# Kernel tuning notes

Measured on AMD Instinct MI355X. Metric: run time of the kernel, lower is better.

## Reference

```python
import jax, jax.numpy as jnp
import numpy as np

B, C, H, W = 32, 384, 32, 32
NCH = 4           # chunks per branch (mixing_size = [4,4,4])
CH = C // NCH     # 96 channels per chunk


def setup_inputs() -> dict:
    key = jax.random.key(0)
    ks = iter(jax.random.split(key, 32))
    r = lambda shape, s=0.05: jax.random.normal(next(ks), shape, dtype=jnp.float32) * s
    inp = {"x": jax.random.normal(next(ks), (B, C, H, W), dtype=jnp.float32)}
    for b, k in zip((1, 2, 3), (1, 3, 5)):
        inp[f"f{b}_mlp_w1"] = r((2, CH, CH // 8))
        inp[f"f{b}_mlp_b1"] = r((2, CH // 8))
        inp[f"f{b}_mlp_w2"] = r((2, CH // 8, CH))
        inp[f"f{b}_mlp_b2"] = r((2, CH))
        inp[f"f{b}_conv_w"] = r((2, CH, 1, k, k))
        inp[f"f{b}_conv_b"] = r((2, CH))
    inp["fusion_w1"] = r((C, C // 4))
    inp["fusion_b1"] = r((C // 4,))
    inp["fusion_w2"] = r((C // 4, 3 * C))
    inp["fusion_b2"] = r((3 * C,))
    inp["proj_w"] = r((C, C))
    inp["proj_b"] = r((C,))
    return inp


def _gelu(x):
    return jax.nn.gelu(x, approximate=False)  # torch nn.GELU default (erf)


def _branch(x, mw1, mb1, mw2, mb2, cw, cb, pad):
    # x: (B, C, H, W); chunks of CH channels; even idx -> MLP (channel-last), odd -> depthwise conv
    chunks = jnp.split(x, NCH, axis=1)
    outs, mi, ci = [], 0, 0
    for i, c in enumerate(chunks):
        if i % 2 == 0:
            h = _gelu(jnp.einsum('bchw,cd->bdhw', c, mw1[mi]) + mb1[mi][:, None, None])
            y = jnp.einsum('bdhw,dc->bchw', h, mw2[mi]) + mb2[mi][:, None, None]
            mi += 1
        else:
            y = jax.lax.conv_general_dilated(
                c, cw[ci], window_strides=(1, 1), padding=[(pad, pad), (pad, pad)],
                feature_group_count=CH, dimension_numbers=('NCHW', 'OIHW', 'NCHW'))
            y = y + cb[ci][:, None, None]
            ci += 1
        outs.append(y)
    return jnp.concatenate(outs, axis=1)


def reference(x,
              f1_mlp_w1, f1_mlp_b1, f1_mlp_w2, f1_mlp_b2, f1_conv_w, f1_conv_b,
              f2_mlp_w1, f2_mlp_b1, f2_mlp_w2, f2_mlp_b2, f2_conv_w, f2_conv_b,
              f3_mlp_w1, f3_mlp_b1, f3_mlp_w2, f3_mlp_b2, f3_conv_w, f3_conv_b,
              fusion_w1, fusion_b1, fusion_w2, fusion_b2, proj_w, proj_b):
    x1 = _branch(x, f1_mlp_w1, f1_mlp_b1, f1_mlp_w2, f1_mlp_b2, f1_conv_w, f1_conv_b, pad=0)
    x2 = _branch(x, f2_mlp_w1, f2_mlp_b1, f2_mlp_w2, f2_mlp_b2, f2_conv_w, f2_conv_b, pad=1)
    x3 = _branch(x, f3_mlp_w1, f3_mlp_b1, f3_mlp_w2, f3_mlp_b2, f3_conv_w, f3_conv_b, pad=2)
    # softmax-gated multi-scale fusion
    a = (x1 + x2 + x3).mean(axis=(2, 3))                            # (B, C)
    g = _gelu(a @ fusion_w1 + fusion_b1) @ fusion_w2 + fusion_b2     # (B, 3C)
    g = g.reshape(a.shape[0], C, 3).transpose(2, 0, 1)               # (3, B, C)
    w = jax.nn.softmax(g, axis=0)[:, :, :, None, None]               # (3, B, C, 1, 1)
    comb = x1 * w[0] + x2 * w[1] + x3 * w[2]                         # (B, C, H, W)
    out = jnp.einsum('bchw,cd->bdhw', comb, proj_w) + proj_b[:, None, None]
    return out
```

## Files before the change

kernel.cpp:

```cpp
#include <hip/hip_runtime.h>
#include <math.h>

#define B_  32
#define C_  384
#define HW  1024

typedef float          f32x4 __attribute__((ext_vector_type(4)));
typedef short          s16x8 __attribute__((ext_vector_type(8)));
typedef unsigned short us8v  __attribute__((ext_vector_type(8)));

struct KParams {
  const float* x;
  const float* mw1[3]; const float* mb1[3]; const float* mw2[3]; const float* mb2[3];
  const float* cw[3];  const float* cb[3];
  const float* fw1; const float* fb1; const float* fw2; const float* fb2;
  const float* pw;  const float* pb;
  float* wg;
  float* H_part;
  float* acv_part;
  unsigned short* pwT;
  float* out;
};

__device__ __forceinline__ float gelu_exact(float v) {
  return 0.5f * v * (1.0f + erff(v * 0.70710678118654752440f));
}
__device__ __forceinline__ unsigned short f2bf(float f) {
  unsigned u = __float_as_uint(f);
  u += 0x7FFFu + ((u >> 16) & 1u);
  return (unsigned short)(u >> 16);
}
__device__ __forceinline__ float bf2f(unsigned short h) {
  return __uint_as_float(((unsigned)h) << 16);
}

__global__ __launch_bounds__(256) void k_prep(KParams P) {
  __shared__ float tile[32][33];
  const int td = blockIdx.x % 12, tc = blockIdx.x / 12;
  const int j = threadIdx.x & 31, i0 = threadIdx.x >> 5;
  const int gcoff = (tc < 3) ? 0 : (tc < 6 ? 96 : (tc < 9 ? -96 : 0));
  for (int i = i0; i < 32; i += 8)
    tile[i][j] = P.pw[(size_t)(tc*32 + i + gcoff)*C_ + td*32 + j];
  __syncthreads();
  for (int i = i0; i < 32; i += 8)
    P.pwT[(size_t)(td*32 + i)*C_ + tc*32 + j] = f2bf(tile[j][i]);
}

template<int HALF>
__device__ __forceinline__ void conv_strip(const float* xc, int h0, int row,
                                           float w1t, const float* w3, const float* w5,
                                           float* y0, float* y1, float* y2) {
#pragma unroll
  for (int p = 0; p < 16; ++p) { y0[p] = 0.f; y1[p] = 0.f; y2[p] = 0.f; }
#pragma unroll
  for (int dy = 0; dy < 5; ++dy) {
    const int hr = h0 + row - 2 + dy;
    float win[20];
    if (hr >= 0 && hr < 32) {
#pragma unroll
      for (int u = 0; u < 5; ++u)
        *(float4*)&win[u*4] = *(const float4*)&xc[hr*32 + HALF*12 + u*4];
    } else {
#pragma unroll
      for (int u = 0; u < 20; ++u) win[u] = 0.f;
    }
#pragma unroll
    for (int dx = 0; dx < 5; ++dx) {
      const float w = w5[dy*5 + dx];
#pragma unroll
      for (int p = 0; p < 16; ++p) {
        const int ri = p + dx - 2 + HALF*4;
        if (ri >= 0 && ri < 20) y2[p] += win[ri] * w;
      }
    }
    if (dy >= 1 && dy <= 3) {
#pragma unroll
      for (int dx = 0; dx < 3; ++dx) {
        const float w = w3[(dy-1)*3 + dx];
#pragma unroll
        for (int p = 0; p < 16; ++p) {
          const int ri = p + dx - 1 + HALF*4;
          if (ri >= 0 && ri < 20) y1[p] += win[ri] * w;
        }
      }
      if (dy == 2) {
#pragma unroll
        for (int p = 0; p < 16; ++p) y0[p] = win[p + HALF*4] * w1t;
      }
    }
  }
}

__global__ __launch_bounds__(256, 2) void k_sum(KParams P) {
  __shared__ __align__(16) char sm[49152 + 13824 + 256];
  const int bid = blockIdx.x;
  const int b = bid >> 5, ci = (bid >> 3) & 3, q = bid & 7;
  const int h0 = q * 4;
  const int t = threadIdx.x;

  if ((ci & 1) == 0) {
    const int mi = ci >> 1;
    float* Xl  = (float*)sm;
    float* w1l = (float*)(sm + 49152);
    float* Hl  = (float*)(sm + 49152 + 13824);
    for (int i = t; i < 3456; i += 256) {
      int s = i / 1152, r = i - s*1152;
      w1l[i] = P.mw1[s][mi*1152 + r];
    }
    for (int i = t*4; i < 12288; i += 1024) {
      int c = i >> 7, pix = i & 127;
      *(float4*)&Xl[i] = *(const float4*)&P.x[(size_t)(b*C_ + mi*192 + c)*HW + h0*32 + pix];
    }
    __syncthreads();
    const int quad = t & 31, sjg = t >> 6;
    const int cq = (t >> 5) & 1;
    const int sj0 = sjg * 9;
    float h[9][4];
#pragma unroll
    for (int u = 0; u < 9; ++u) { h[u][0]=0.f; h[u][1]=0.f; h[u][2]=0.f; h[u][3]=0.f; }
    int wbase[9];
#pragma unroll
    for (int u = 0; u < 9; ++u) {
      int sj = sj0 + u, s = sj / 12, jj = sj % 12;
      wbase[u] = s*1152 + jj;
    }
    for (int c = cq*48; c < cq*48 + 48; ++c) {
      const float4 xv = *(const float4*)&Xl[c*128 + quad*4];
#pragma unroll
      for (int u = 0; u < 9; ++u) {
        const float w = w1l[wbase[u] + c*12];
        h[u][0] += xv.x*w; h[u][1] += xv.y*w; h[u][2] += xv.z*w; h[u][3] += xv.w*w;
      }
    }
#pragma unroll
    for (int u = 0; u < 9; ++u)
#pragma unroll
      for (int p = 0; p < 4; ++p) h[u][p] += __shfl_xor(h[u][p], 32, 64);
    float hs[9];
#pragma unroll
    for (int u = 0; u < 9; ++u) {
      int sj = sj0 + u, s = sj / 12, jj = sj % 12;
      const float bias = P.mb1[s][mi*12 + jj];
      float sum = 0.f;
#pragma unroll
      for (int p = 0; p < 4; ++p) sum += gelu_exact(h[u][p] + bias);
#pragma unroll
      for (int m = 16; m >= 1; m >>= 1) sum += __shfl_xor(sum, m, 64);
      hs[u] = sum;
    }
    if ((t & 63) == 0) {
#pragma unroll
      for (int u = 0; u < 9; ++u) Hl[sj0 + u] = hs[u];
    }
    __syncthreads();
    if (t < 36) P.H_part[(size_t)((b*2 + mi)*8 + q)*36 + t] = Hl[t];
  } else {
    const int gi = ci >> 1;
    float* accl = (float*)sm;
    if (t < 96) accl[t] = 0.f;
    __syncthreads();
    for (int it = 0; it < 2; ++it) {
      const int task = t + 256*it;
      if (task < 384) {
        const int row = task & 3, cc = task >> 2;
        const int gcl = gi*96 + cc;
        const float* xc = P.x + (size_t)(b*C_ + (2*gi+1)*96 + cc)*HW;
        const float w1t = P.cw[0][gcl];
        float w3[9], w5[25];
#pragma unroll
        for (int k2 = 0; k2 < 9; ++k2)  w3[k2] = P.cw[1][gcl*9 + k2];
#pragma unroll
        for (int k2 = 0; k2 < 25; ++k2) w5[k2] = P.cw[2][gcl*25 + k2];
        float val = 0.f;
        {
          float y0[16], y1[16], y2[16];
          conv_strip<0>(xc, h0, row, w1t, w3, w5, y0, y1, y2);
#pragma unroll
          for (int p = 0; p < 16; ++p) val += y0[p] + y1[p] + y2[p];
          conv_strip<1>(xc, h0, row, w1t, w3, w5, y0, y1, y2);
#pragma unroll
          for (int p = 0; p < 16; ++p) val += y0[p] + y1[p] + y2[p];
        }
        atomicAdd(&accl[cc], val);
      }
    }
    __syncthreads();
    if (t < 96) P.acv_part[(size_t)((b*2 + gi)*8 + q)*96 + t] = accl[t];
  }
}

__global__ __launch_bounds__(128) void k_gate(KParams P) {
  const int b = blockIdx.x, t = threadIdx.x;
  __shared__ float am[C_], g1v[96], Hs[2][36];
  for (int i = t; i < 72; i += 128) {
    int mi = i / 36, sj = i % 36;
    float s = 0.f;
    for (int q = 0; q < 8; ++q) s += P.H_part[(size_t)((b*2+mi)*8 + q)*36 + sj];
    Hs[mi][sj] = s * (1.0f/1024.0f);
  }
  __syncthreads();
  for (int i = t; i < 192; i += 128) {
    int mi = i / 96, cc = i % 96;
    float a = 0.f;
    for (int s = 0; s < 3; ++s) {
      float y = P.mb2[s][mi*96 + cc];
      for (int jj = 0; jj < 12; ++jj) y += Hs[mi][s*12+jj] * P.mw2[s][mi*1152 + jj*96 + cc];
      a += y;
    }
    am[mi*192 + cc] = a;
  }
  for (int i = t; i < 192; i += 128) {
    int gi = i / 96, cc = i % 96;
    float s = 0.f;
    for (int q = 0; q < 8; ++q) s += P.acv_part[(size_t)((b*2+gi)*8 + q)*96 + cc];
    s *= (1.0f/1024.0f);
    for (int sb = 0; sb < 3; ++sb) s += P.cb[sb][gi*96 + cc];
    am[(2*gi+1)*96 + cc] = s;
  }
  __syncthreads();
  if (t < 96) {
    float acc = P.fb1[t];
    for (int c = 0; c < C_; ++c) acc += am[c] * P.fw1[c*96 + t];
    g1v[t] = gelu_exact(acc);
  }
  __syncthreads();
  for (int c = t; c < C_; c += 128) {
    float l0 = P.fb2[c*3+0], l1 = P.fb2[c*3+1], l2 = P.fb2[c*3+2];
    for (int jj = 0; jj < 96; ++jj) {
      const float g = g1v[jj];
      const float* f = P.fw2 + jj*1152 + c*3;
      l0 += g*f[0]; l1 += g*f[1]; l2 += g*f[2];
    }
    const float m = fmaxf(l0, fmaxf(l1, l2));
    const float e0 = expf(l0-m), e1 = expf(l1-m), e2 = expf(l2-m);
    const float inv = 1.0f/(e0+e1+e2);
    P.wg[0*(B_*C_) + b*C_ + c] = e0*inv;
    P.wg[1*(B_*C_) + b*C_ + c] = e1*inv;
    P.wg[2*(B_*C_) + b*C_ + c] = e2*inv;
  }
}

template<int HALF>
__device__ __forceinline__ void conv_phase(const KParams& P, int b, int h0,
                                           char* combB, const float* wgl, int tt) {
  for (int it = 0; it < 3; ++it) {
    const int tid = tt + 256*it;
    const int row = tid & 3, c192 = tid >> 2;
    const int gi = c192 / 96, cc = c192 - gi*96;
    const int gcl = gi*96 + cc;
    const int gc = (2*gi + 1)*96 + cc;
    const int kp = 192 + gi*96 + cc;
    const float* xc = P.x + (size_t)(b*C_ + gc)*HW;
    const float w1t = P.cw[0][gcl];
    float w3[9], w5[25];
#pragma unroll
    for (int k2 = 0; k2 < 9; ++k2)  w3[k2] = P.cw[1][gcl*9 + k2];
#pragma unroll
    for (int k2 = 0; k2 < 25; ++k2) w5[k2] = P.cw[2][gcl*25 + k2];
    float y0[16], y1[16], y2[16];
    conv_strip<HALF>(xc, h0, row, w1t, w3, w5, y0, y1, y2);
    const float g0 = wgl[0*C_ + gc], g1 = wgl[1*C_ + gc], g2 = wgl[2*C_ + gc];
    const float cbg = g0*P.cb[0][gcl] + g1*P.cb[1][gcl] + g2*P.cb[2][gcl];
#pragma unroll
    for (int p = 0; p < 16; ++p) {
      const float v = g0*y0[p] + g1*y1[p] + g2*y2[p] + cbg;
      const int pix = row*32 + HALF*16 + p;
      const int off = pix*768 + (((kp*2)) ^ ((pix & 15) << 4));
      *(unsigned short*)(combB + off) = f2bf(v);
    }
  }
}

__global__ __launch_bounds__(512, 1) void k_proj(KParams P) {
  __shared__ __align__(16) char smem[159744];
  char* combB = smem;
  char* hlB   = smem + 98304;
  char* XB    = smem + 116736;
  unsigned short* wlB = (unsigned short*)(smem + 141312);
  float* wgl  = (float*)(smem + 155136);

  const int t = threadIdx.x;
  const int b  = blockIdx.x >> 3;
  const int h0 = (blockIdx.x & 7) * 4;

  for (int i = t; i < 1152; i += 512)
    wgl[i] = P.wg[(size_t)(i/C_)*(B_*C_) + b*C_ + (i % C_)];
  for (int i = t; i < 6912; i += 512) {
    int s = i / 2304, r = i - s*2304, mi2 = r / 1152, rr = r - mi2*1152;
    wlB[i] = f2bf(P.mw1[s][mi2*1152 + rr]);
  }
  for (int i = t*4; i < 12288; i += 2048) {
    int c = i >> 7, pix = i & 127;
    float4 v = *(const float4*)&P.x[(size_t)(b*C_ + 0*192 + c)*HW + h0*32 + pix];
    unsigned lo = (unsigned)f2bf(v.x) | ((unsigned)f2bf(v.y) << 16);
    unsigned hi = (unsigned)f2bf(v.z) | ((unsigned)f2bf(v.w) << 16);
    *(uint2*)(XB + c*256 + pix*2) = make_uint2(lo, hi);
  }
  __syncthreads();

#pragma unroll 1
  for (int mi = 0; mi < 2; ++mi) {
    if (t < 256) {
      const int oct = t & 15, cq = (t >> 4) & 1, sjg = t >> 5;
      const int nsj = (sjg < 4) ? 5 : 4;
      const int sj0 = (sjg < 4) ? sjg*5 : 20 + (sjg - 4)*4;
      int wbase[5]; float bias[5];
#pragma unroll
      for (int u = 0; u < 5; ++u) {
        int sj = sj0 + ((u < 5 && u < nsj) ? u : 0);
        int s = sj / 12, jj = sj - s*12;
        wbase[u] = (s*2 + mi)*1152 + jj;
        bias[u] = P.mb1[s][mi*12 + jj];
      }
      float h[5][8];
#pragma unroll
      for (int u = 0; u < 5; ++u)
#pragma unroll
        for (int p = 0; p < 8; ++p) h[u][p] = 0.f;
      for (int c = cq*48; c < cq*48 + 48; ++c) {
        const us8v xv = *(const us8v*)(XB + c*256 + oct*16);
        float xf[8];
#pragma unroll
        for (int p = 0; p < 8; ++p) xf[p] = bf2f(xv[p]);
#pragma unroll
        for (int u = 0; u < 5; ++u) {
          if (u < nsj) {
            const float w = bf2f(wlB[wbase[u] + c*12]);
#pragma unroll
            for (int p = 0; p < 8; ++p) h[u][p] += xf[p]*w;
          }
        }
      }
#pragma unroll
      for (int u = 0; u < 5; ++u)
#pragma unroll
        for (int p = 0; p < 8; ++p) h[u][p] += __shfl_xor(h[u][p], 16, 64);
      if (cq == 0) {
#pragma unroll
        for (int u = 0; u < 5; ++u) {
          if (u < nsj) {
            us8v o;
#pragma unroll
            for (int p = 0; p < 8; ++p) o[p] = f2bf(gelu_exact(h[u][p] + bias[u]));
            *(us8v*)(hlB + (mi*36 + sj0 + u)*256 + oct*16) = o;
          }
        }
      }
    } else {
      if (mi == 0) conv_phase<0>(P, b, h0, combB, wgl, t - 256);
      else         conv_phase<1>(P, b, h0, combB, wgl, t - 256);
    }
    __syncthreads();
    if (mi == 0) {
      for (int i = t*4; i < 12288; i += 2048) {
        int c = i >> 7, pix = i & 127;
        float4 v = *(const float4*)&P.x[(size_t)(b*C_ + 192 + c)*HW + h0*32 + pix];
        unsigned lo = (unsigned)f2bf(v.x) | ((unsigned)f2bf(v.y) << 16);
        unsigned hi = (unsigned)f2bf(v.z) | ((unsigned)f2bf(v.w) << 16);
        *(uint2*)(XB + c*256 + pix*2) = make_uint2(lo, hi);
      }
      __syncthreads();
    }
  }

  for (int i = t; i < 6912; i += 512) {
    int s = i / 2304, r = i - s*2304, mi2 = r / 1152, rr = r - mi2*1152;
    wlB[i] = f2bf(P.mw2[s][mi2*1152 + rr]);
  }
  __syncthreads();

  {
    const int ct = t & 15, pt = (t >> 4) & 15, mi = t >> 8;
    const int c0 = ct*6, pix0 = pt*8;
    float wgc[3][6];
#pragma unroll
    for (int s = 0; s < 3; ++s)
#pragma unroll
      for (int i = 0; i < 6; ++i) wgc[s][i] = wgl[s*C_ + mi*192 + c0 + i];
    float acc[6][8];
#pragma unroll
    for (int i = 0; i < 6; ++i) {
      float ai = 0.f;
#pragma unroll
      for (int s = 0; s < 3; ++s) ai += wgc[s][i] * P.mb2[s][mi*96 + c0 + i];
#pragma unroll
      for (int p = 0; p < 8; ++p) acc[i][p] = ai;
    }
#pragma unroll
    for (int s = 0; s < 3; ++s)
#pragma unroll
      for (int jj = 0; jj < 12; ++jj) {
        const us8v hv = *(const us8v*)(hlB + (mi*36 + s*12 + jj)*256 + pix0*2);
        float hf[8];
#pragma unroll
        for (int p = 0; p < 8; ++p) hf[p] = bf2f(hv[p]);
        const unsigned short* wp = wlB + (s*2 + mi)*1152 + jj*96 + c0;
        float gw[6];
#pragma unroll
        for (int i = 0; i < 6; ++i) gw[i] = bf2f(wp[i]) * wgc[s][i];
#pragma unroll
        for (int i = 0; i < 6; ++i)
#pragma unroll
          for (int p = 0; p < 8; ++p) acc[i][p] += gw[i]*hf[p];
      }
#pragma unroll
    for (int i = 0; i < 6; ++i)
#pragma unroll
      for (int p = 0; p < 8; ++p) {
        const int pix = pix0 + p;
        const int kp2 = mi*96 + c0 + i;
        const int off = pix*768 + ((kp2*2) ^ ((pix & 15) << 4));
        *(unsigned short*)(combB + off) = f2bf(acc[i][p]);
      }
  }
  __syncthreads();

  {
    const int lane = t & 63, wv = t >> 6;
    const int wm = wv & 1, wn = wv >> 1;
    const int l15 = lane & 15, l4 = lane >> 4;
    f32x4 acc[4][6];
#pragma unroll
    for (int mt = 0; mt < 4; ++mt)
#pragma unroll
      for (int nt = 0; nt < 6; ++nt) acc[mt][nt] = (f32x4){0.f,0.f,0.f,0.f};
    const char* pwTb = (const char*)P.pwT;
#pragma unroll 2
    for (int ks = 0; ks < 12; ++ks) {
      const int k0 = ks*32 + l4*8;
      s16x8 af[4], bfr[6];
#pragma unroll
      for (int mt = 0; mt < 4; ++mt) {
        const int m = wm*64 + mt*16 + l15;
        af[mt] = *(const s16x8*)(combB + m*768 + ((2*k0) ^ ((m & 15) << 4)));
      }
#pragma unroll
      for (int nt = 0; nt < 6; ++nt) {
        const int d = wn*96 + nt*16 + l15;
        bfr[nt] = *(const s16x8*)(pwTb + (size_t)d*768 + 2*k0);
      }
#pragma unroll
      for (int mt = 0; mt < 4; ++mt)
#pragma unroll
        for (int nt = 0; nt < 6; ++nt)
          acc[mt][nt] = __builtin_amdgcn_mfma_f32_16x16x32_bf16(af[mt], bfr[nt], acc[mt][nt], 0, 0, 0);
    }
#pragma unroll
    for (int nt = 0; nt < 6; ++nt) {
      const int d = wn*96 + nt*16 + l15;
      const float pbv = P.pb[d];
#pragma unroll
      for (int mt = 0; mt < 4; ++mt) {
        const int pix = wm*64 + mt*16 + l4*4;
        float4 o;
        o.x = acc[mt][nt][0] + pbv;
        o.y = acc[mt][nt][1] + pbv;
        o.z = acc[mt][nt][2] + pbv;
        o.w = acc[mt][nt][3] + pbv;
        *(float4*)&P.out[(size_t)(b*C_ + d)*HW + (h0 + (pix >> 5))*32 + (pix & 31)] = o;
      }
    }
  }
}

extern "C" void kernel_launch(void* const* d_in, const int* in_sizes, int n_in,
                              void* d_out, int out_size, void* d_ws, size_t ws_size,
                              hipStream_t stream) {
  KParams P;
  P.x = (const float*)d_in[0];
  for (int s = 0; s < 3; ++s) {
    const int base = 1 + s * 6;
    P.mw1[s] = (const float*)d_in[base + 0];
    P.mb1[s] = (const float*)d_in[base + 1];
    P.mw2[s] = (const float*)d_in[base + 2];
    P.mb2[s] = (const float*)d_in[base + 3];
    P.cw[s]  = (const float*)d_in[base + 4];
    P.cb[s]  = (const float*)d_in[base + 5];
  }
  P.fw1 = (const float*)d_in[19]; P.fb1 = (const float*)d_in[20];
  P.fw2 = (const float*)d_in[21]; P.fb2 = (const float*)d_in[22];
  P.pw  = (const float*)d_in[23]; P.pb  = (const float*)d_in[24];
  float* w = (float*)d_ws;
  P.wg       = w;
  P.H_part   = w + 36864;
  P.acv_part = w + 55296;
  P.pwT      = (unsigned short*)(w + 104448);
  P.out = (float*)d_out;

  k_prep<<<144, 256, 0, stream>>>(P);
  k_sum <<<1024, 256, 0, stream>>>(P);
  k_gate<<<32, 128, 0, stream>>>(P);
  k_proj<<<256, 512, 0, stream>>>(P);
}
```

Measured before the change: 280.1 us.

## Derive conv-branch spatial means from boundary sums and widen proj to 1024 threads

The sum pass no longer runs the three depthwise convolutions just to get channel means. It now computes per-channel totals plus first/last row and column partial sums and corner pixels, and k_gate rebuilds each padded convolution's mean algebraically from these boundary terms. k_proj moves from 512 to 1024 threads with the MLP, conv and MFMA work split finer per thread, and k_gate uses 256 threads with a split fw1 reduction. The changes add global atomics and a memset of the accumulator workspace, and the 1024-thread k_proj may be limited by registers.

```diff
diff --git a/kernel.cpp b/kernel.cpp
--- a/kernel.cpp
+++ b/kernel.cpp
@@ -17,7 +17,8 @@
   const float* pw;  const float* pb;
   float* wg;
   float* H_part;
-  float* acv_part;
+  float* cvA;
+  float* ext;
   unsigned short* pwT;
   float* out;
 };
@@ -94,12 +95,12 @@
 __global__ __launch_bounds__(256, 2) void k_sum(KParams P) {
   __shared__ __align__(16) char sm[49152 + 13824 + 256];
   const int bid = blockIdx.x;
-  const int b = bid >> 5, ci = (bid >> 3) & 3, q = bid & 7;
-  const int h0 = q * 4;
+  const int b = bid >> 5, sub = bid & 31;
   const int t = threadIdx.x;
 
-  if ((ci & 1) == 0) {
-    const int mi = ci >> 1;
+  if (sub < 16) {
+    const int mi = sub >> 3, q = sub & 7;
+    const int h0 = q * 4;
     float* Xl  = (float*)sm;
     float* w1l = (float*)(sm + 49152);
     float* Hl  = (float*)(sm + 49152 + 13824);
@@ -155,51 +156,67 @@
     __syncthreads();
     if (t < 36) P.H_part[(size_t)((b*2 + mi)*8 + q)*36 + t] = Hl[t];
   } else {
-    const int gi = ci >> 1;
-    float* accl = (float*)sm;
-    if (t < 96) accl[t] = 0.f;
-    __syncthreads();
-    for (int it = 0; it < 2; ++it) {
-      const int task = t + 256*it;
-      if (task < 384) {
-        const int row = task & 3, cc = task >> 2;
-        const int gcl = gi*96 + cc;
-        const float* xc = P.x + (size_t)(b*C_ + (2*gi+1)*96 + cc)*HW;
-        const float w1t = P.cw[0][gcl];
-        float w3[9], w5[25];
-#pragma unroll
-        for (int k2 = 0; k2 < 9; ++k2)  w3[k2] = P.cw[1][gcl*9 + k2];
-#pragma unroll
-        for (int k2 = 0; k2 < 25; ++k2) w5[k2] = P.cw[2][gcl*25 + k2];
-        float val = 0.f;
-        {
-          float y0[16], y1[16], y2[16];
-          conv_strip<0>(xc, h0, row, w1t, w3, w5, y0, y1, y2);
-#pragma unroll
-          for (int p = 0; p < 16; ++p) val += y0[p] + y1[p] + y2[p];
-          conv_strip<1>(xc, h0, row, w1t, w3, w5, y0, y1, y2);
-#pragma unroll
-          for (int p = 0; p < 16; ++p) val += y0[p] + y1[p] + y2[p];
+    const int s2 = sub - 16;
+    const int gi = s2 >> 3, q = s2 & 7;
+    const int h0 = q * 4;
+    const int lane = t & 63, wv = t >> 6;
+    const int gcbase = (2*gi + 1) * 96;
+    for (int i = 0; i < 24; ++i) {
+      const int cc = wv*24 + i;
+      const float* xc = P.x + (size_t)(b*C_ + gcbase + cc)*HW + h0*32;
+      const float2 v = *(const float2*)(xc + 2*lane);
+      const float t2 = v.x + v.y;
+      float T = t2;
+      T += __shfl_xor(T, 1, 64);  T += __shfl_xor(T, 2, 64);
+      T += __shfl_xor(T, 4, 64);  T += __shfl_xor(T, 8, 64);
+      T += __shfl_xor(T, 16, 64); T += __shfl_xor(T, 32, 64);
+      float c0  = ((lane & 15) == 0)  ? v.x : 0.f;
+      float c1  = ((lane & 15) == 0)  ? v.y : 0.f;
+      float c30 = ((lane & 15) == 15) ? v.x : 0.f;
+      float c31 = ((lane & 15) == 15) ? v.y : 0.f;
+      c0  += __shfl_xor(c0, 16, 64);  c0  += __shfl_xor(c0, 32, 64);
+      c1  += __shfl_xor(c1, 16, 64);  c1  += __shfl_xor(c1, 32, 64);
+      c30 += __shfl_xor(c30, 16, 64); c30 += __shfl_xor(c30, 32, 64);
+      c31 += __shfl_xor(c31, 16, 64); c31 += __shfl_xor(c31, 32, 64);
+      if (lane == 0) {
+        float* A = &P.cvA[(size_t)(b*2 + gi)*5*96 + cc];
+        atomicAdd(A + 0*96, T);   atomicAdd(A + 1*96, c0);
+        atomicAdd(A + 2*96, c1);  atomicAdd(A + 3*96, c30);
+        atomicAdd(A + 4*96, c31);
+      }
+      if (q == 0 || q == 7) {
+        float r = t2;
+        r += __shfl_xor(r, 1, 64); r += __shfl_xor(r, 2, 64);
+        r += __shfl_xor(r, 4, 64); r += __shfl_xor(r, 8, 64);
+        const int e  = (q == 0) ? 0 : 1;
+        const int lo = (q == 0) ? 0 : 32;
+        const float Ra  = __shfl(r,   lo,      64), Rb  = __shfl(r,   lo + 16, 64);
+        const float p00 = __shfl(v.x, lo,      64), p01 = __shfl(v.y, lo,      64);
+        const float p0a = __shfl(v.x, lo + 15, 64), p0b = __shfl(v.y, lo + 15, 64);
+        const float p10 = __shfl(v.x, lo + 16, 64), p11 = __shfl(v.y, lo + 16, 64);
+        const float p1a = __shfl(v.x, lo + 31, 64), p1b = __shfl(v.y, lo + 31, 64);
+        if (lane == 0) {
+          float* E = &P.ext[((size_t)(b*2 + gi)*2 + e)*10*96 + cc];
+          E[0*96] = Ra;  E[1*96] = Rb;
+          E[2*96] = p00; E[3*96] = p01; E[4*96] = p0a; E[5*96] = p0b;
+          E[6*96] = p10; E[7*96] = p11; E[8*96] = p1a; E[9*96] = p1b;
         }
-        atomicAdd(&accl[cc], val);
-      }
-    }
-    __syncthreads();
-    if (t < 96) P.acv_part[(size_t)((b*2 + gi)*8 + q)*96 + t] = accl[t];
-  }
-}
-
-__global__ __launch_bounds__(128) void k_gate(KParams P) {
+      }
+    }
+  }
+}
+
+__global__ __launch_bounds__(256) void k_gate(KParams P) {
   const int b = blockIdx.x, t = threadIdx.x;
-  __shared__ float am[C_], g1v[96], Hs[2][36];
-  for (int i = t; i < 72; i += 128) {
+  __shared__ float am[C_], g1p[2][96], g1v[96], Hs[2][36];
+  for (int i = t; i < 72; i += 256) {
     int mi = i / 36, sj = i % 36;
     float s = 0.f;
     for (int q = 0; q < 8; ++q) s += P.H_part[(size_t)((b*2+mi)*8 + q)*36 + sj];
     Hs[mi][sj] = s * (1.0f/1024.0f);
   }
   __syncthreads();
-  for (int i = t; i < 192; i += 128) {
+  for (int i = t; i < 192; i += 256) {
     int mi = i / 96, cc = i % 96;
     float a = 0.f;
     for (int s = 0; s < 3; ++s) {
@@ -209,22 +226,63 @@
     }
     am[mi*192 + cc] = a;
   }
-  for (int i = t; i < 192; i += 128) {
-    int gi = i / 96, cc = i % 96;
-    float s = 0.f;
-    for (int q = 0; q < 8; ++q) s += P.acv_part[(size_t)((b*2+gi)*8 + q)*96 + cc];
-    s *= (1.0f/1024.0f);
-    for (int sb = 0; sb < 3; ++sb) s += P.cb[sb][gi*96 + cc];
-    am[(2*gi+1)*96 + cc] = s;
-  }
-  __syncthreads();
-  if (t < 96) {
-    float acc = P.fb1[t];
-    for (int c = 0; c < C_; ++c) acc += am[c] * P.fw1[c*96 + t];
-    g1v[t] = gelu_exact(acc);
-  }
-  __syncthreads();
-  for (int c = t; c < C_; c += 128) {
+  for (int i = t; i < 192; i += 256) {
+    const int gi = i / 96, cc = i % 96;
+    const float* A  = &P.cvA[(size_t)(b*2 + gi)*5*96 + cc];
+    const float T   = A[0*96];
+    const float C0  = A[1*96], C1  = A[2*96], C30 = A[3*96], C31 = A[4*96];
+    const float* E0 = &P.ext[((size_t)(b*2 + gi)*2 + 0)*10*96 + cc];
+    const float* E1 = &P.ext[((size_t)(b*2 + gi)*2 + 1)*10*96 + cc];
+    const float R0  = E0[0*96], R1  = E0[1*96];
+    const float a00 = E0[2*96], a01 = E0[3*96], a0a = E0[4*96], a0b = E0[5*96];
+    const float a10 = E0[6*96], a11 = E0[7*96], a1a = E0[8*96], a1b = E0[9*96];
+    const float R30 = E1[0*96], R31 = E1[1*96];
+    const float b00 = E1[2*96], b01 = E1[3*96], b0a = E1[4*96], b0b = E1[5*96];
+    const float b10 = E1[6*96], b11 = E1[7*96], b1a = E1[8*96], b1b = E1[9*96];
+    const float ER[5]   = {R30+R31, R31, 0.f, R0, R0+R1};
+    const float EC[5]   = {C30+C31, C31, 0.f, C0, C0+C1};
+    const float cr0[5]  = {a0a+a0b, a0b, 0.f, a00, a00+a01};
+    const float cr1[5]  = {a1a+a1b, a1b, 0.f, a10, a10+a11};
+    const float cr30[5] = {b0a+b0b, b0b, 0.f, b00, b00+b01};
+    const float cr31[5] = {b1a+b1b, b1b, 0.f, b10, b10+b11};
+    const int gcl = gi*96 + cc;
+    float sum = P.cw[0][gcl] * T;
+#pragma unroll
+    for (int dy = 0; dy < 3; ++dy)
+#pragma unroll
+      for (int dx = 0; dx < 3; ++dx) {
+        const int s = dy - 1, u = dx - 1;
+        float xc_ = 0.f;
+        if (s == 1)  xc_ = cr0[u+2];
+        if (s == -1) xc_ = cr31[u+2];
+        sum += P.cw[1][gcl*9 + dy*3 + dx] * (T - ER[s+2] - EC[u+2] + xc_);
+      }
+#pragma unroll
+    for (int dy = 0; dy < 5; ++dy)
+#pragma unroll
+      for (int dx = 0; dx < 5; ++dx) {
+        const int s = dy - 2, u = dx - 2;
+        float xc_ = 0.f;
+        if (s == 1)  xc_ = cr0[u+2];
+        if (s == 2)  xc_ = cr0[u+2] + cr1[u+2];
+        if (s == -1) xc_ = cr31[u+2];
+        if (s == -2) xc_ = cr30[u+2] + cr31[u+2];
+        sum += P.cw[2][gcl*25 + dy*5 + dx] * (T - ER[s+2] - EC[u+2] + xc_);
+      }
+    am[(2*gi+1)*96 + cc] = sum * (1.0f/1024.0f)
+                         + P.cb[0][gcl] + P.cb[1][gcl] + P.cb[2][gcl];
+  }
+  __syncthreads();
+  if (t < 192) {
+    const int jj = t % 96, half = t / 96;
+    float acc = 0.f;
+    for (int c = half*192; c < half*192 + 192; ++c) acc += am[c] * P.fw1[c*96 + jj];
+    g1p[half][jj] = acc;
+  }
+  __syncthreads();
+  if (t < 96) g1v[t] = gelu_exact(g1p[0][t] + g1p[1][t] + P.fb1[t]);
+  __syncthreads();
+  for (int c = t; c < C_; c += 256) {
     float l0 = P.fb2[c*3+0], l1 = P.fb2[c*3+1], l2 = P.fb2[c*3+2];
     for (int jj = 0; jj < 96; ++jj) {
       const float g = g1v[jj];
@@ -241,37 +299,39 @@
 }
 
 template<int HALF>
-__device__ __forceinline__ void conv_phase(const KParams& P, int b, int h0,
-                                           char* combB, const float* wgl, int tt) {
-  for (int it = 0; it < 3; ++it) {
-    const int tid = tt + 256*it;
-    const int row = tid & 3, c192 = tid >> 2;
-    const int gi = c192 / 96, cc = c192 - gi*96;
-    const int gcl = gi*96 + cc;
-    const int gc = (2*gi + 1)*96 + cc;
-    const int kp = 192 + gi*96 + cc;
-    const float* xc = P.x + (size_t)(b*C_ + gc)*HW;
-    const float w1t = P.cw[0][gcl];
-    float w3[9], w5[25];
-#pragma unroll
-    for (int k2 = 0; k2 < 9; ++k2)  w3[k2] = P.cw[1][gcl*9 + k2];
-#pragma unroll
-    for (int k2 = 0; k2 < 25; ++k2) w5[k2] = P.cw[2][gcl*25 + k2];
-    float y0[16], y1[16], y2[16];
-    conv_strip<HALF>(xc, h0, row, w1t, w3, w5, y0, y1, y2);
-    const float g0 = wgl[0*C_ + gc], g1 = wgl[1*C_ + gc], g2 = wgl[2*C_ + gc];
-    const float cbg = g0*P.cb[0][gcl] + g1*P.cb[1][gcl] + g2*P.cb[2][gcl];
-#pragma unroll
-    for (int p = 0; p < 16; ++p) {
-      const float v = g0*y0[p] + g1*y1[p] + g2*y2[p] + cbg;
-      const int pix = row*32 + HALF*16 + p;
-      const int off = pix*768 + (((kp*2)) ^ ((pix & 15) << 4));
-      *(unsigned short*)(combB + off) = f2bf(v);
-    }
-  }
-}
-
-__global__ __launch_bounds__(512, 1) void k_proj(KParams P) {
+__device__ __forceinline__ void conv_phase2(const KParams& P, int b, int h0,
+                                            char* combB, const float* wgl, int tt) {
+  for (int it = 0; it < 2; ++it) {
+    const int task = tt + 512*it;
+    if (task < 768) {
+      const int row = task & 3, c192 = task >> 2;
+      const int gi = c192 / 96, cc = c192 - gi*96;
+      const int gcl = gi*96 + cc;
+      const int gc = (2*gi + 1)*96 + cc;
+      const int kp = 192 + gi*96 + cc;
+      const float* xc = P.x + (size_t)(b*C_ + gc)*HW;
+      const float w1t = P.cw[0][gcl];
+      float w3[9], w5[25];
+#pragma unroll
+      for (int k2 = 0; k2 < 9; ++k2)  w3[k2] = P.cw[1][gcl*9 + k2];
+#pragma unroll
+      for (int k2 = 0; k2 < 25; ++k2) w5[k2] = P.cw[2][gcl*25 + k2];
+      float y0[16], y1[16], y2[16];
+      conv_strip<HALF>(xc, h0, row, w1t, w3, w5, y0, y1, y2);
+      const float g0 = wgl[0*C_ + gc], g1 = wgl[1*C_ + gc], g2 = wgl[2*C_ + gc];
+      const float cbg = g0*P.cb[0][gcl] + g1*P.cb[1][gcl] + g2*P.cb[2][gcl];
+#pragma unroll
+      for (int p = 0; p < 16; ++p) {
+        const float v = g0*y0[p] + g1*y1[p] + g2*y2[p] + cbg;
+        const int pix = row*32 + HALF*16 + p;
+        const int off = pix*768 + ((kp*2) ^ ((pix & 15) << 4));
+        *(unsigned short*)(combB + off) = f2bf(v);
+      }
+    }
+  }
+}
+
+__global__ __launch_bounds__(1024) void k_proj(KParams P) {
   __shared__ __align__(16) char smem[159744];
   char* combB = smem;
   char* hlB   = smem + 98304;
@@ -279,19 +339,19 @@
   unsigned short* wlB = (unsigned short*)(smem + 141312);
   float* wgl  = (float*)(smem + 155136);
 
-  const int t = threadIdx.x;
+  const int t  = threadIdx.x;
   const int b  = blockIdx.x >> 3;
   const int h0 = (blockIdx.x & 7) * 4;
 
-  for (int i = t; i < 1152; i += 512)
+  for (int i = t; i < 1152; i += 1024)
     wgl[i] = P.wg[(size_t)(i/C_)*(B_*C_) + b*C_ + (i % C_)];
-  for (int i = t; i < 6912; i += 512) {
+  for (int i = t; i < 6912; i += 1024) {
     int s = i / 2304, r = i - s*2304, mi2 = r / 1152, rr = r - mi2*1152;
     wlB[i] = f2bf(P.mw1[s][mi2*1152 + rr]);
   }
-  for (int i = t*4; i < 12288; i += 2048) {
+  for (int i = t*4; i < 12288; i += 4096) {
     int c = i >> 7, pix = i & 127;
-    float4 v = *(const float4*)&P.x[(size_t)(b*C_ + 0*192 + c)*HW + h0*32 + pix];
+    float4 v = *(const float4*)&P.x[(size_t)(b*C_ + c)*HW + h0*32 + pix];
     unsigned lo = (unsigned)f2bf(v.x) | ((unsigned)f2bf(v.y) << 16);
     unsigned hi = (unsigned)f2bf(v.z) | ((unsigned)f2bf(v.w) << 16);
     *(uint2*)(XB + c*256 + pix*2) = make_uint2(lo, hi);
@@ -300,14 +360,14 @@
 
 #pragma unroll 1
   for (int mi = 0; mi < 2; ++mi) {
-    if (t < 256) {
-      const int oct = t & 15, cq = (t >> 4) & 1, sjg = t >> 5;
+    if (t < 512) {
+      const int oct = t & 15, cq = (t >> 4) & 3, sjg = t >> 6;
       const int nsj = (sjg < 4) ? 5 : 4;
       const int sj0 = (sjg < 4) ? sjg*5 : 20 + (sjg - 4)*4;
       int wbase[5]; float bias[5];
 #pragma unroll
       for (int u = 0; u < 5; ++u) {
-        int sj = sj0 + ((u < 5 && u < nsj) ? u : 0);
+        int sj = sj0 + ((u < nsj) ? u : 0);
         int s = sj / 12, jj = sj - s*12;
         wbase[u] = (s*2 + mi)*1152 + jj;
         bias[u] = P.mb1[s][mi*12 + jj];
@@ -317,7 +377,7 @@
       for (int u = 0; u < 5; ++u)
 #pragma unroll
         for (int p = 0; p < 8; ++p) h[u][p] = 0.f;
-      for (int c = cq*48; c < cq*48 + 48; ++c) {
+      for (int c = cq*24; c < cq*24 + 24; ++c) {
         const us8v xv = *(const us8v*)(XB + c*256 + oct*16);
         float xf[8];
 #pragma unroll
@@ -334,7 +394,10 @@
 #pragma unroll
       for (int u = 0; u < 5; ++u)
 #pragma unroll
-        for (int p = 0; p < 8; ++p) h[u][p] += __shfl_xor(h[u][p], 16, 64);
+        for (int p = 0; p < 8; ++p) {
+          h[u][p] += __shfl_xor(h[u][p], 16, 64);
+          h[u][p] += __shfl_xor(h[u][p], 32, 64);
+        }
       if (cq == 0) {
 #pragma unroll
         for (int u = 0; u < 5; ++u) {
@@ -347,12 +410,12 @@
         }
       }
     } else {
-      if (mi == 0) conv_phase<0>(P, b, h0, combB, wgl, t - 256);
-      else         conv_phase<1>(P, b, h0, combB, wgl, t - 256);
+      if (mi == 0) conv_phase2<0>(P, b, h0, combB, wgl, t - 512);
+      else         conv_phase2<1>(P, b, h0, combB, wgl, t - 512);
     }
     __syncthreads();
     if (mi == 0) {
-      for (int i = t*4; i < 12288; i += 2048) {
+      for (int i = t*4; i < 12288; i += 4096) {
         int c = i >> 7, pix = i & 127;
         float4 v = *(const float4*)&P.x[(size_t)(b*C_ + 192 + c)*HW + h0*32 + pix];
         unsigned lo = (unsigned)f2bf(v.x) | ((unsigned)f2bf(v.y) << 16);
@@ -363,23 +426,23 @@
     }
   }
 
-  for (int i = t; i < 6912; i += 512) {
+  for (int i = t; i < 6912; i += 1024) {
     int s = i / 2304, r = i - s*2304, mi2 = r / 1152, rr = r - mi2*1152;
     wlB[i] = f2bf(P.mw2[s][mi2*1152 + rr]);
   }
   __syncthreads();
 
   {
-    const int ct = t & 15, pt = (t >> 4) & 15, mi = t >> 8;
-    const int c0 = ct*6, pix0 = pt*8;
-    float wgc[3][6];
+    const int ct = t & 31, pt = (t >> 5) & 15, mi = t >> 9;
+    const int c0 = ct*3, pix0 = pt*8;
+    float wgc[3][3];
 #pragma unroll
     for (int s = 0; s < 3; ++s)
 #pragma unroll
-      for (int i = 0; i < 6; ++i) wgc[s][i] = wgl[s*C_ + mi*192 + c0 + i];
-    float acc[6][8];
-#pragma unroll
-    for (int i = 0; i < 6; ++i) {
+      for (int i = 0; i < 3; ++i) wgc[s][i] = wgl[s*C_ + mi*192 + c0 + i];
+    float acc[3][8];
+#pragma unroll
+    for (int i = 0; i < 3; ++i) {
       float ai = 0.f;
 #pragma unroll
       for (int s = 0; s < 3; ++s) ai += wgc[s][i] * P.mb2[s][mi*96 + c0 + i];
@@ -395,16 +458,16 @@
 #pragma unroll
         for (int p = 0; p < 8; ++p) hf[p] = bf2f(hv[p]);
         const unsigned short* wp = wlB + (s*2 + mi)*1152 + jj*96 + c0;
-        float gw[6];
-#pragma unroll
-        for (int i = 0; i < 6; ++i) gw[i] = bf2f(wp[i]) * wgc[s][i];
-#pragma unroll
-        for (int i = 0; i < 6; ++i)
+        float gw[3];
+#pragma unroll
+        for (int i = 0; i < 3; ++i) gw[i] = bf2f(wp[i]) * wgc[s][i];
+#pragma unroll
+        for (int i = 0; i < 3; ++i)
 #pragma unroll
           for (int p = 0; p < 8; ++p) acc[i][p] += gw[i]*hf[p];
       }
 #pragma unroll
-    for (int i = 0; i < 6; ++i)
+    for (int i = 0; i < 3; ++i)
 #pragma unroll
       for (int p = 0; p < 8; ++p) {
         const int pix = pix0 + p;
@@ -419,35 +482,35 @@
     const int lane = t & 63, wv = t >> 6;
     const int wm = wv & 1, wn = wv >> 1;
     const int l15 = lane & 15, l4 = lane >> 4;
-    f32x4 acc[4][6];
+    f32x4 acc[4][3];
 #pragma unroll
     for (int mt = 0; mt < 4; ++mt)
 #pragma unroll
-      for (int nt = 0; nt < 6; ++nt) acc[mt][nt] = (f32x4){0.f,0.f,0.f,0.f};
+      for (int nt = 0; nt < 3; ++nt) acc[mt][nt] = (f32x4){0.f,0.f,0.f,0.f};
     const char* pwTb = (const char*)P.pwT;
 #pragma unroll 2
     for (int ks = 0; ks < 12; ++ks) {
       const int k0 = ks*32 + l4*8;
-      s16x8 af[4], bfr[6];
+      s16x8 af[4], bfr[3];
 #pragma unroll
       for (int mt = 0; mt < 4; ++mt) {
         const int m = wm*64 + mt*16 + l15;
         af[mt] = *(const s16x8*)(combB + m*768 + ((2*k0) ^ ((m & 15) << 4)));
       }
 #pragma unroll
-      for (int nt = 0; nt < 6; ++nt) {
-        const int d = wn*96 + nt*16 + l15;
+      for (int nt = 0; nt < 3; ++nt) {
+        const int d = wn*48 + nt*16 + l15;
         bfr[nt] = *(const s16x8*)(pwTb + (size_t)d*768 + 2*k0);
       }
 #pragma unroll
       for (int mt = 0; mt < 4; ++mt)
 #pragma unroll
-        for (int nt = 0; nt < 6; ++nt)
+        for (int nt = 0; nt < 3; ++nt)
           acc[mt][nt] = __builtin_amdgcn_mfma_f32_16x16x32_bf16(af[mt], bfr[nt], acc[mt][nt], 0, 0, 0);
     }
 #pragma unroll
-    for (int nt = 0; nt < 6; ++nt) {
-      const int d = wn*96 + nt*16 + l15;
+    for (int nt = 0; nt < 3; ++nt) {
+      const int d = wn*48 + nt*16 + l15;
       const float pbv = P.pb[d];
 #pragma unroll
       for (int mt = 0; mt < 4; ++mt) {
@@ -481,14 +544,16 @@
   P.fw2 = (const float*)d_in[21]; P.fb2 = (const float*)d_in[22];
   P.pw  = (const float*)d_in[23]; P.pb  = (const float*)d_in[24];
   float* w = (float*)d_ws;
-  P.wg       = w;
-  P.H_part   = w + 36864;
-  P.acv_part = w + 55296;
-  P.pwT      = (unsigned short*)(w + 104448);
+  P.wg     = w;
+  P.H_part = w + 36864;
+  P.cvA    = w + 55296;
+  P.ext    = w + 86016;
+  P.pwT    = (unsigned short*)(w + 208896);
   P.out = (float*)d_out;
 
+  hipMemsetAsync((char*)d_ws + 55296*sizeof(float), 0, 30720*sizeof(float), stream);
   k_prep<<<144, 256, 0, stream>>>(P);
   k_sum <<<1024, 256, 0, stream>>>(P);
-  k_gate<<<32, 128, 0, stream>>>(P);
-  k_proj<<<256, 512, 0, stream>>>(P);
-}
+  k_gate<<<32, 256, 0, stream>>>(P);
+  k_proj<<<256, 1024, 0, stream>>>(P);
+}
```

After: 304.9 us. +8.9%, slower.
